# Optimization experiments

Measured on AMD Instinct MI355X. Metric: run time of the kernel, lower is better.

## Reference

```python
import jax, jax.numpy as jnp
import numpy as np

NUM_ATOMS = 50000
NUM_EDGES = 200000  # even: edges come in (fwd, rev) pairs
D_V, D_E, D_H = 133, 14, 256
DEPTH = 3


def setup_inputs() -> dict:
    key = jax.random.key(0)
    ks = jax.random.split(key, 12)
    half = NUM_EDGES // 2
    src = jax.random.randint(ks[0], (half,), 0, NUM_ATOMS)
    dst = jax.random.randint(ks[1], (half,), 0, NUM_ATOMS)
    v = jnp.concatenate([src, dst])
    w = jnp.concatenate([dst, src])
    edge_index = jnp.stack([v, w])  # [2, E]
    rev_edge_index = jnp.concatenate([jnp.arange(half) + half, jnp.arange(half)])

    def lin(k, out_d, in_d):
        return jax.random.normal(k, (out_d, in_d), jnp.float32) / np.sqrt(in_d)

    return {
        "V": jax.random.normal(ks[2], (NUM_ATOMS, D_V), jnp.float32),
        "E_feat": jax.random.normal(ks[3], (NUM_EDGES, D_E), jnp.float32),
        "edge_index": edge_index,
        "rev_edge_index": rev_edge_index,
        "Wi_atom": lin(ks[4], D_H, D_V),
        "Wi_bond": lin(ks[5], D_H, D_V + D_E),
        "Wh_atom": lin(ks[6], D_H, D_H),
        "Wh_bond": lin(ks[7], D_H, D_H),
        "Wf_atom": lin(ks[8], D_H, D_H),
        "Wf_bond": lin(ks[9], D_H, D_H),
        "Wo_atom": lin(ks[10], D_H, D_V + D_H),
    }


def _sum_and_max_into_atoms(H_e, w_idx, num_atoms):
    a_sum = jax.ops.segment_sum(H_e, w_idx, num_segments=num_atoms)
    a_max = jax.ops.segment_max(H_e, w_idx, num_segments=num_atoms)
    a_max = jnp.where(jnp.isfinite(a_max), a_max, 0.0)  # empty segments -> 0
    return a_sum, a_max


def _fuse(H, m, Wf):
    # Fusion(kind='mlp', residual=True), dropout=0:
    # residual update with a small MLP on the combined signal
    return H + jax.nn.relu((H + m) @ Wf.T)


def reference(V, E_feat, edge_index, rev_edge_index, Wi_atom, Wi_bond,
              Wh_atom, Wh_bond, Wf_atom, Wf_bond, Wo_atom):
    tau = jax.nn.relu
    num_atoms = V.shape[0]
    v = edge_index[0]
    w = edge_index[1]

    H_a = tau(V @ Wi_atom.T)                                        # [N, d_h]
    H_b = tau(jnp.concatenate([V[v], E_feat], axis=1) @ Wi_bond.T)  # [E, d_h]

    for _ in range(1, DEPTH):
        a_sum, a_max = _sum_and_max_into_atoms(H_b, w, num_atoms)
        gate = a_sum * a_max
        m_a = gate @ Wh_atom.T
        H_a = _fuse(H_a, m_a, Wf_atom)

        M_b = a_sum[v] - H_b[rev_edge_index]
        m_b = M_b @ Wh_bond.T
        H_b = _fuse(H_b, m_b, Wf_bond)

    a_sum, _ = _sum_and_max_into_atoms(H_b, w, num_atoms)
    H_atom = tau(jnp.concatenate([V, a_sum], axis=1) @ Wo_atom.T)   # [N, d_h]
    return H_atom
```

## Files before the change

### kernel.cpp

```cpp
#include <hip/hip_runtime.h>
#include <hip/hip_bf16.h>

#define NATOM 50000
#define NEDGE 200000
#define HALF  100000
#define DV    133
#define DE    14
#define DH    256
#define KVP   160
#define NBLK_SCAN ((NATOM + 255) / 256)

typedef __bf16  bf16x8 __attribute__((ext_vector_type(8)));
typedef __bf16  bf16x4 __attribute__((ext_vector_type(4)));
typedef float   f32x4  __attribute__((ext_vector_type(4)));

enum { EPI_RELU = 0, EPI_ADDBASE = 1, EPI_FUSE = 2, EPI_NONE = 3, EPI_RELUADD = 4 };
enum { AM_PLAIN = 0, AM_GATE = 1, AM_GDIFF = 2, AM_VF32 = 3, AM_XB = 4, AM_F32 = 5 };

__device__ __forceinline__ void gll16(const void* g, void* l) {
    __builtin_amdgcn_global_load_lds(
        (const __attribute__((address_space(1))) unsigned int*)g,
        (__attribute__((address_space(3))) unsigned int*)l, 16, 0, 0);
}
__device__ __forceinline__ void drain_barrier() {
    __builtin_amdgcn_s_waitcnt(0);
    __syncthreads();
}

struct GArgs {
    const __bf16* A; int lda;
    const float* asumf; const __bf16* amaxb;
    const __bf16* HbG; const int* vidx; const int* rev;
    const float* Vf; const float* Ef;
    const __bf16* W; int ldw;
    const __bf16* base; __bf16* C; float* Cf;
    int Mloc; int part0; int off0; int off1;
};

template<int AMODE, int EPI, int CLOC, int STF32, int KITERS>
__global__ __launch_bounds__(256, 2) void gemm128(GArgs g, int nblk) {
    __shared__ __bf16 Alds[4096];
    __shared__ __bf16 Blds[4096];
    const int tid  = threadIdx.x;
    const int lane = tid & 63, wv = tid >> 6;
    const int quad = lane >> 4, l16 = lane & 15;
    const int wr = (wv >> 1) * 64, wc = (wv & 1) * 64;
    const int lrow = lane >> 2, lu = lane & 3;

    for (int blk = blockIdx.x; blk < nblk; blk += gridDim.x) {
        const int ch = blk >> 1, half = blk & 1;
        const int gr0  = ch * 128;
        const int colb = half * 128;

        const int rs = tid >> 1, seg = tid & 1;
        const float *sp = nullptr; const __bf16 *hp = nullptr, *mp = nullptr;
        const float *vp = nullptr, *ep = nullptr;
        if (AMODE != AM_PLAIN) {
            int grs = gr0 + rs; if (grs > g.Mloc - 1) grs = g.Mloc - 1;
            const int maps = (grs < g.part0) ? g.off0 + grs : g.off1 + grs - g.part0;
            if (AMODE == AM_GATE)  { sp = g.asumf + (size_t)maps * DH; mp = g.amaxb + (size_t)maps * DH; }
            if (AMODE == AM_GDIFF) { sp = g.asumf + (size_t)g.vidx[maps] * DH; hp = g.HbG + (size_t)g.rev[maps] * DH; }
            if (AMODE == AM_F32)   { sp = g.asumf + (size_t)maps * DH; }
            if (AMODE == AM_VF32)  { vp = g.Vf + (size_t)maps * DV; }
            if (AMODE == AM_XB)    { vp = g.Vf + (size_t)g.vidx[maps] * DV; ep = g.Ef + (size_t)maps * DE; }
        }

        f32x4 acc[16];
#pragma unroll
        for (int i = 0; i < 16; ++i) acc[i] = (f32x4){0.f, 0.f, 0.f, 0.f};

        for (int kk = 0; kk < KITERS; ++kk) {
#pragma unroll
            for (int s = 0; s < 2; ++s) {
                int cl = (wv * 2 + s) * 16 + lrow;
                gll16(g.W + (size_t)(colb + cl) * g.ldw + kk * 32 + lu * 8,
                      Blds + (wv * 2 + s) * 512);
            }
            if (AMODE == AM_PLAIN) {
#pragma unroll
                for (int s = 0; s < 2; ++s) {
                    int r = (wv * 2 + s) * 16 + lrow;
                    int gra = gr0 + r; if (gra > g.Mloc - 1) gra = g.Mloc - 1;
                    gll16(g.A + (size_t)gra * g.lda + kk * 32 + lu * 8,
                          Alds + (wv * 2 + s) * 512);
                }
            } else {
                bf16x8 o0, o1;
                const int cb = kk * 32 + seg * 16;
                if (AMODE == AM_GATE || AMODE == AM_GDIFF || AMODE == AM_F32) {
                    f32x4 s0 = *(const f32x4*)(sp + cb);
                    f32x4 s1 = *(const f32x4*)(sp + cb + 4);
                    f32x4 s2 = *(const f32x4*)(sp + cb + 8);
                    f32x4 s3 = *(const f32x4*)(sp + cb + 12);
                    if (AMODE == AM_GATE) {
                        bf16x8 m0 = *(const bf16x8*)(mp + cb);
                        bf16x8 m1 = *(const bf16x8*)(mp + cb + 8);
#pragma unroll
                        for (int j = 0; j < 4; ++j) {
                            o0[j]     = (__bf16)(s0[j] * (float)m0[j]);
                            o0[4 + j] = (__bf16)(s1[j] * (float)m0[4 + j]);
                            o1[j]     = (__bf16)(s2[j] * (float)m1[j]);
                            o1[4 + j] = (__bf16)(s3[j] * (float)m1[4 + j]);
                        }
                    } else if (AMODE == AM_GDIFF) {
                        bf16x8 h0 = *(const bf16x8*)(hp + cb);
                        bf16x8 h1 = *(const bf16x8*)(hp + cb + 8);
#pragma unroll
                        for (int j = 0; j < 4; ++j) {
                            o0[j]     = (__bf16)(s0[j] - (float)h0[j]);
                            o0[4 + j] = (__bf16)(s1[j] - (float)h0[4 + j]);
                            o1[j]     = (__bf16)(s2[j] - (float)h1[j]);
                            o1[4 + j] = (__bf16)(s3[j] - (float)h1[4 + j]);
                        }
                    } else {
#pragma unroll
                        for (int j = 0; j < 4; ++j) {
                            o0[j]     = (__bf16)s0[j];
                            o0[4 + j] = (__bf16)s1[j];
                            o1[j]     = (__bf16)s2[j];
                            o1[4 + j] = (__bf16)s3[j];
                        }
                    }
                } else {
                    if (kk < 4) {
                        f32x4 x0, x1, x2, x3;
                        __builtin_memcpy(&x0, vp + cb, 16);
                        __builtin_memcpy(&x1, vp + cb + 4, 16);
                        __builtin_memcpy(&x2, vp + cb + 8, 16);
                        __builtin_memcpy(&x3, vp + cb + 12, 16);
#pragma unroll
                        for (int j = 0; j < 4; ++j) {
                            o0[j] = (__bf16)x0[j]; o0[4 + j] = (__bf16)x1[j];
                            o1[j] = (__bf16)x2[j]; o1[4 + j] = (__bf16)x3[j];
                        }
                    } else {
#pragma unroll
                        for (int j = 0; j < 8; ++j) {
                            int c0 = cb + j, c1 = cb + 8 + j;
                            float y0 = 0.f, y1 = 0.f;
                            if (c0 < DV) y0 = vp[c0];
                            else if (AMODE == AM_XB && c0 < DV + DE) y0 = ep[c0 - DV];
                            if (c1 < DV) y1 = vp[c1];
                            else if (AMODE == AM_XB && c1 < DV + DE) y1 = ep[c1 - DV];
                            o0[j] = (__bf16)y0; o1[j] = (__bf16)y1;
                        }
                    }
                }
                *(bf16x8*)(Alds + rs * 32 + seg * 16)     = o0;
                *(bf16x8*)(Alds + rs * 32 + seg * 16 + 8) = o1;
            }
            drain_barrier();

            bf16x8 af[4], bfv[4];
#pragma unroll
            for (int m = 0; m < 4; ++m)
                af[m] = *(const bf16x8*)(Alds + (wr + m * 16 + l16) * 32 + quad * 8);
#pragma unroll
            for (int n = 0; n < 4; ++n)
                bfv[n] = *(const bf16x8*)(Blds + (wc + n * 16 + l16) * 32 + quad * 8);
#pragma unroll
            for (int m = 0; m < 4; ++m)
#pragma unroll
                for (int n = 0; n < 4; ++n)
                    acc[m * 4 + n] = __builtin_amdgcn_mfma_f32_16x16x32_bf16(
                        af[m], bfv[n], acc[m * 4 + n], 0, 0, 0);
            drain_barrier();
        }

#pragma unroll
        for (int m = 0; m < 4; ++m)
#pragma unroll
        for (int n = 0; n < 4; ++n)
#pragma unroll
        for (int r = 0; r < 4; ++r) {
            int gr = gr0 + wr + m * 16 + quad * 4 + r;
            if (gr < g.Mloc) {
                int mapped = (gr < g.part0) ? g.off0 + gr : g.off1 + gr - g.part0;
                int crow = CLOC ? gr : mapped;
                int col = colb + wc + n * 16 + l16;
                size_t co = (size_t)crow * DH + col;
                float v = acc[m * 4 + n][r];
                float res;
                if (EPI == EPI_RELU)       res = v > 0.f ? v : 0.f;
                else if (EPI == EPI_NONE)  res = v;
                else {
                    float b = (float)g.base[(size_t)mapped * DH + col];
                    if (EPI == EPI_ADDBASE)      res = b + v;
                    else if (EPI == EPI_FUSE)    res = b + (v > 0.f ? v : 0.f);
                    else        { res = b + v; res = res > 0.f ? res : 0.f; }
                }
                if (STF32) g.Cf[co] = res;
                else       g.C[co]  = (__bf16)res;
            }
        }
    }
}

__global__ void count_deg(const int* __restrict__ widx, int* __restrict__ cnt) {
    int e = blockIdx.x * 256 + threadIdx.x;
    if (e < NEDGE) atomicAdd(&cnt[widx[e]], 1);
}

__global__ __launch_bounds__(256) void scan_p1(const int* __restrict__ cnt,
                                               int* __restrict__ rowptr,
                                               int* __restrict__ bsum) {
    __shared__ int sm[256];
    const int tid = threadIdx.x;
    const int i = blockIdx.x * 256 + tid;
    int v = (i < NATOM) ? cnt[i] : 0;
    sm[tid] = v;
    __syncthreads();
    for (int off = 1; off < 256; off <<= 1) {
        int t = (tid >= off) ? sm[tid - off] : 0;
        __syncthreads();
        sm[tid] += t;
        __syncthreads();
    }
    if (i < NATOM) rowptr[i] = sm[tid] - v;
    if (tid == 255) bsum[blockIdx.x] = sm[255];
}

__global__ __launch_bounds__(256) void scan_p2(int* __restrict__ bsum) {
    __shared__ int sm[256];
    const int tid = threadIdx.x;
    int v = (tid < NBLK_SCAN) ? bsum[tid] : 0;
    sm[tid] = v;
    __syncthreads();
    for (int off = 1; off < 256; off <<= 1) {
        int t = (tid >= off) ? sm[tid - off] : 0;
        __syncthreads();
        sm[tid] += t;
        __syncthreads();
    }
    if (tid < NBLK_SCAN) bsum[tid] = sm[tid] - v;
    if (tid == 255) bsum[NBLK_SCAN] = sm[255];
}

__global__ __launch_bounds__(256) void scan_p3(int* __restrict__ rowptr,
                                               int* __restrict__ cursor,
                                               const int* __restrict__ bsum) {
    const int i = blockIdx.x * 256 + threadIdx.x;
    if (i < NATOM) {
        int r = rowptr[i] + bsum[blockIdx.x];
        rowptr[i] = r;
        cursor[i] = r;
    }
    if (i == 0) rowptr[NATOM] = bsum[NBLK_SCAN];
}

__global__ void fill_csr(const int* __restrict__ widx, int* __restrict__ cursor,
                         int* __restrict__ eid) {
    int e = blockIdx.x * 256 + threadIdx.x;
    if (e >= NEDGE) return;
    int pos = atomicAdd(&cursor[widx[e]], 1);
    eid[pos] = e;
}

template<int WITHMAX>
__global__ __launch_bounds__(256) void seg_reduce(
    const __bf16* __restrict__ Hb, const int* __restrict__ rowptr,
    const int* __restrict__ eid,
    float* __restrict__ asum, __bf16* __restrict__ amaxb)
{
    int a = blockIdx.x * 4 + (threadIdx.x >> 6);
    if (a >= NATOM) return;
    const int lane = threadIdx.x & 63;
    const int beg = rowptr[a], end = rowptr[a + 1];
    float s0 = 0.f, s1 = 0.f, s2 = 0.f, s3 = 0.f;
    float m0 = 0.f, m1 = 0.f, m2 = 0.f, m3 = 0.f;
    for (int i = beg; i < end; ++i) {
        int e = eid[i];
        bf16x4 h = *(const bf16x4*)(Hb + (size_t)e * DH + lane * 4);
        float v0 = (float)h[0], v1 = (float)h[1], v2 = (float)h[2], v3 = (float)h[3];
        s0 += v0; s1 += v1; s2 += v2; s3 += v3;
        if (WITHMAX) {
            m0 = fmaxf(m0, v0); m1 = fmaxf(m1, v1);
            m2 = fmaxf(m2, v2); m3 = fmaxf(m3, v3);
        }
    }
    size_t o = (size_t)a * DH + lane * 4;
    *(f32x4*)(asum + o) = (f32x4){s0, s1, s2, s3};
    if (WITHMAX) {
        bf16x4 mv; mv[0] = (__bf16)m0; mv[1] = (__bf16)m1; mv[2] = (__bf16)m2; mv[3] = (__bf16)m3;
        *(bf16x4*)(amaxb + o) = mv;
    }
}

__global__ void pad_w2(const float* __restrict__ src, __bf16* __restrict__ dst,
                       int srcld, int coloff, int KS, int KD) {
    int i = blockIdx.x * 256 + threadIdx.x;
    if (i >= 256 * KD) return;
    int n = i / KD, c = i - n * KD;
    dst[i] = (c < KS) ? (__bf16)src[(size_t)n * srcld + coloff + c] : (__bf16)0.f;
}

static inline int cdiv(long a, long b) { return (int)((a + b - 1) / b); }
static inline int gsz2(int nblk) { return nblk < 2048 ? nblk : 2048; }

extern "C" void kernel_launch(void* const* d_in, const int* in_sizes, int n_in,
                              void* d_out, int out_size, void* d_ws, size_t ws_size,
                              hipStream_t stream) {
    const float* V    = (const float*)d_in[0];
    const float* Ef   = (const float*)d_in[1];
    const int*   ei   = (const int*)d_in[2];
    const int*   rev  = (const int*)d_in[3];
    const float* Wi_a = (const float*)d_in[4];
    const float* Wi_b = (const float*)d_in[5];
    const float* Wh_a = (const float*)d_in[6];
    const float* Wh_b = (const float*)d_in[7];
    const float* Wf_a = (const float*)d_in[8];
    const float* Wf_b = (const float*)d_in[9];
    const float* Wo   = (const float*)d_in[10];
    float* out = (float*)d_out;

    const int* vidx = ei;
    const int* widx = ei + NEDGE;

    char* ws = (char*)d_ws;
    __bf16* Hb    = (__bf16*)(ws + 0);
    __bf16* Ha    = (__bf16*)(ws + 102400000);
    char*   S     = ws + 128000000;
    float*  asum  = (float*)(ws + 192000000);
    __bf16* amaxb = (__bf16*)(S + 0);
    __bf16* Ta    = (__bf16*)(S + 25600000);
    __bf16* Tb    = (__bf16*)(S + 0);
    __bf16* T     = (__bf16*)(S + 25600000);
    __bf16* Wia   = (__bf16*)(ws + 243200000);
    __bf16* Wib   = (__bf16*)(ws + 243281920);
    __bf16* Wo1   = (__bf16*)(ws + 243363840);
    __bf16* Wo2   = (__bf16*)(ws + 243445760);
    __bf16* Wha   = (__bf16*)(ws + 243576832);
    __bf16* Whb   = (__bf16*)(ws + 243707904);
    __bf16* Wfa   = (__bf16*)(ws + 243838976);
    __bf16* Wfb   = (__bf16*)(ws + 243970048);
    int*  rowptr  = (int*)(ws + 244101120);
    int*  cursor  = (int*)(ws + 244301312);
    int*  eid     = (int*)(ws + 244501504);
    int*  bsum    = (int*)(ws + 128000000);
    (void)ws_size;

    hipMemsetAsync(cursor, 0, NATOM * sizeof(int), stream);
    count_deg<<<cdiv(NEDGE, 256), 256, 0, stream>>>(widx, cursor);
    scan_p1<<<NBLK_SCAN, 256, 0, stream>>>(cursor, rowptr, bsum);
    scan_p2<<<1, 256, 0, stream>>>(bsum);
    scan_p3<<<NBLK_SCAN, 256, 0, stream>>>(rowptr, cursor, bsum);
    fill_csr<<<cdiv(NEDGE, 256), 256, 0, stream>>>(widx, cursor, eid);

    pad_w2<<<cdiv(256 * KVP, 256), 256, 0, stream>>>(Wi_a, Wia, DV, 0, DV, KVP);
    pad_w2<<<cdiv(256 * KVP, 256), 256, 0, stream>>>(Wi_b, Wib, DV + DE, 0, DV + DE, KVP);
    pad_w2<<<cdiv(256 * KVP, 256), 256, 0, stream>>>(Wo, Wo1, DV + DH, 0, DV, KVP);
    pad_w2<<<cdiv(256 * DH, 256), 256, 0, stream>>>(Wo, Wo2, DV + DH, DV, DH, DH);
    pad_w2<<<cdiv(256 * DH, 256), 256, 0, stream>>>(Wh_a, Wha, DH, 0, DH, DH);
    pad_w2<<<cdiv(256 * DH, 256), 256, 0, stream>>>(Wh_b, Whb, DH, 0, DH, DH);
    pad_w2<<<cdiv(256 * DH, 256), 256, 0, stream>>>(Wf_a, Wfa, DH, 0, DH, DH);
    pad_w2<<<cdiv(256 * DH, 256), 256, 0, stream>>>(Wf_b, Wfb, DH, 0, DH, DH);

    GArgs ga{};
    ga.asumf = asum; ga.amaxb = amaxb; ga.HbG = Hb; ga.vidx = vidx; ga.rev = rev;
    ga.Vf = V; ga.Ef = Ef;

    {
        int nblk = cdiv(NATOM, 128) * 2;
        ga.W = Wia; ga.ldw = KVP; ga.C = Ha;
        ga.Mloc = NATOM; ga.part0 = NATOM; ga.off0 = 0; ga.off1 = 0;
        gemm128<AM_VF32, EPI_RELU, 0, 0, 5><<<gsz2(nblk), 256, 0, stream>>>(ga, nblk);
    }
    {
        int nblk = cdiv(NEDGE, 128) * 2;
        ga.W = Wib; ga.ldw = KVP; ga.C = Hb;
        ga.Mloc = NEDGE; ga.part0 = NEDGE; ga.off0 = 0; ga.off1 = 0;
        gemm128<AM_XB, EPI_RELU, 0, 0, 5><<<gsz2(nblk), 256, 0, stream>>>(ga, nblk);
    }

    for (int it = 0; it < 2; ++it) {
        seg_reduce<1><<<cdiv(NATOM, 4), 256, 0, stream>>>(Hb, rowptr, eid, asum, amaxb);

        {
            int nblk = cdiv(NATOM, 128) * 2;
            ga.W = Wha; ga.ldw = DH; ga.base = Ha; ga.C = Ta;
            ga.Mloc = NATOM; ga.part0 = NATOM; ga.off0 = 0; ga.off1 = 0;
            gemm128<AM_GATE, EPI_ADDBASE, 1, 0, 8><<<gsz2(nblk), 256, 0, stream>>>(ga, nblk);
            ga.A = Ta; ga.lda = DH; ga.W = Wfa; ga.base = Ha; ga.C = Ha;
            gemm128<AM_PLAIN, EPI_FUSE, 0, 0, 8><<<gsz2(nblk), 256, 0, stream>>>(ga, nblk);
        }

        for (int c = 0; c < 2; ++c) {
            int nblk = cdiv(HALF, 128) * 2;
            ga.W = Whb; ga.ldw = DH; ga.base = Hb; ga.C = Tb;
            ga.Mloc = HALF; ga.part0 = HALF / 2; ga.off0 = c * 50000; ga.off1 = HALF + c * 50000;
            gemm128<AM_GDIFF, EPI_ADDBASE, 1, 0, 8><<<gsz2(nblk), 256, 0, stream>>>(ga, nblk);
            ga.A = Tb; ga.lda = DH; ga.W = Wfb; ga.base = Hb; ga.C = Hb;
            gemm128<AM_PLAIN, EPI_FUSE, 0, 0, 8><<<gsz2(nblk), 256, 0, stream>>>(ga, nblk);
        }
    }

    seg_reduce<0><<<cdiv(NATOM, 4), 256, 0, stream>>>(Hb, rowptr, eid, asum, nullptr);
    {
        int nblk = cdiv(NATOM, 128) * 2;
        ga.Mloc = NATOM; ga.part0 = NATOM; ga.off0 = 0; ga.off1 = 0;
        ga.W = Wo1; ga.ldw = KVP; ga.C = T;
        gemm128<AM_VF32, EPI_NONE, 0, 0, 5><<<gsz2(nblk), 256, 0, stream>>>(ga, nblk);
        ga.W = Wo2; ga.ldw = DH; ga.base = T; ga.Cf = out;
        gemm128<AM_F32, EPI_RELUADD, 0, 1, 8><<<gsz2(nblk), 256, 0, stream>>>(ga, nblk);
    }
}
```

Measured before the change: 1.206 ms.

## Widen GEMM tile to full 256 output columns with 512-thread blocks

The GEMM kernel now uses 512-thread blocks that compute a 128x256 tile, covering every output column, instead of two 128x128 half tiles per row chunk. Each A row is therefore gathered and converted once rather than twice, which halves the redundant gather/gate/diff work and the A-side global traffic. The cost is a larger B shared-memory tile and bigger blocks, which may lower occupancy and leave fewer blocks to spread across the GPU.

New measurement: 1.204 ms. About the same (-0.1%).

```diff
diff --git a/kernel.cpp b/kernel.cpp
--- a/kernel.cpp
+++ b/kernel.cpp
@@ -38,21 +38,19 @@
 };
 
 template<int AMODE, int EPI, int CLOC, int STF32, int KITERS>
-__global__ __launch_bounds__(256, 2) void gemm128(GArgs g, int nblk) {
+__global__ __launch_bounds__(512, 2) void gemmk(GArgs g, int nblk) {
     __shared__ __bf16 Alds[4096];
-    __shared__ __bf16 Blds[4096];
+    __shared__ __bf16 Blds[8192];
     const int tid  = threadIdx.x;
     const int lane = tid & 63, wv = tid >> 6;
     const int quad = lane >> 4, l16 = lane & 15;
-    const int wr = (wv >> 1) * 64, wc = (wv & 1) * 64;
+    const int wr = (wv >> 2) * 64, wc = (wv & 3) * 64;
     const int lrow = lane >> 2, lu = lane & 3;
 
     for (int blk = blockIdx.x; blk < nblk; blk += gridDim.x) {
-        const int ch = blk >> 1, half = blk & 1;
-        const int gr0  = ch * 128;
-        const int colb = half * 128;
-
-        const int rs = tid >> 1, seg = tid & 1;
+        const int gr0 = blk * 128;
+
+        const int rs = tid >> 2, seg = tid & 3;
         const float *sp = nullptr; const __bf16 *hp = nullptr, *mp = nullptr;
         const float *vp = nullptr, *ep = nullptr;
         if (AMODE != AM_PLAIN) {
@@ -73,81 +71,62 @@
 #pragma unroll
             for (int s = 0; s < 2; ++s) {
                 int cl = (wv * 2 + s) * 16 + lrow;
-                gll16(g.W + (size_t)(colb + cl) * g.ldw + kk * 32 + lu * 8,
+                gll16(g.W + (size_t)cl * g.ldw + kk * 32 + lu * 8,
                       Blds + (wv * 2 + s) * 512);
             }
             if (AMODE == AM_PLAIN) {
-#pragma unroll
-                for (int s = 0; s < 2; ++s) {
-                    int r = (wv * 2 + s) * 16 + lrow;
-                    int gra = gr0 + r; if (gra > g.Mloc - 1) gra = g.Mloc - 1;
-                    gll16(g.A + (size_t)gra * g.lda + kk * 32 + lu * 8,
-                          Alds + (wv * 2 + s) * 512);
-                }
+                int r = wv * 16 + lrow;
+                int gra = gr0 + r; if (gra > g.Mloc - 1) gra = g.Mloc - 1;
+                gll16(g.A + (size_t)gra * g.lda + kk * 32 + lu * 8,
+                      Alds + wv * 512);
             } else {
-                bf16x8 o0, o1;
-                const int cb = kk * 32 + seg * 16;
+                bf16x8 o0;
+                const int cb = kk * 32 + seg * 8;
                 if (AMODE == AM_GATE || AMODE == AM_GDIFF || AMODE == AM_F32) {
                     f32x4 s0 = *(const f32x4*)(sp + cb);
                     f32x4 s1 = *(const f32x4*)(sp + cb + 4);
-                    f32x4 s2 = *(const f32x4*)(sp + cb + 8);
-                    f32x4 s3 = *(const f32x4*)(sp + cb + 12);
                     if (AMODE == AM_GATE) {
                         bf16x8 m0 = *(const bf16x8*)(mp + cb);
-                        bf16x8 m1 = *(const bf16x8*)(mp + cb + 8);
 #pragma unroll
                         for (int j = 0; j < 4; ++j) {
                             o0[j]     = (__bf16)(s0[j] * (float)m0[j]);
                             o0[4 + j] = (__bf16)(s1[j] * (float)m0[4 + j]);
-                            o1[j]     = (__bf16)(s2[j] * (float)m1[j]);
-                            o1[4 + j] = (__bf16)(s3[j] * (float)m1[4 + j]);
                         }
                     } else if (AMODE == AM_GDIFF) {
                         bf16x8 h0 = *(const bf16x8*)(hp + cb);
-                        bf16x8 h1 = *(const bf16x8*)(hp + cb + 8);
 #pragma unroll
                         for (int j = 0; j < 4; ++j) {
                             o0[j]     = (__bf16)(s0[j] - (float)h0[j]);
                             o0[4 + j] = (__bf16)(s1[j] - (float)h0[4 + j]);
-                            o1[j]     = (__bf16)(s2[j] - (float)h1[j]);
-                            o1[4 + j] = (__bf16)(s3[j] - (float)h1[4 + j]);
                         }
                     } else {
 #pragma unroll
                         for (int j = 0; j < 4; ++j) {
                             o0[j]     = (__bf16)s0[j];
                             o0[4 + j] = (__bf16)s1[j];
-                            o1[j]     = (__bf16)s2[j];
-                            o1[4 + j] = (__bf16)s3[j];
                         }
                     }
                 } else {
                     if (kk < 4) {
-                        f32x4 x0, x1, x2, x3;
+                        f32x4 x0, x1;
                         __builtin_memcpy(&x0, vp + cb, 16);
                         __builtin_memcpy(&x1, vp + cb + 4, 16);
-                        __builtin_memcpy(&x2, vp + cb + 8, 16);
-                        __builtin_memcpy(&x3, vp + cb + 12, 16);
 #pragma unroll
                         for (int j = 0; j < 4; ++j) {
                             o0[j] = (__bf16)x0[j]; o0[4 + j] = (__bf16)x1[j];
-                            o1[j] = (__bf16)x2[j]; o1[4 + j] = (__bf16)x3[j];
                         }
                     } else {
 #pragma unroll
                         for (int j = 0; j < 8; ++j) {
-                            int c0 = cb + j, c1 = cb + 8 + j;
-                            float y0 = 0.f, y1 = 0.f;
+                            int c0 = cb + j;
+                            float y0 = 0.f;
                             if (c0 < DV) y0 = vp[c0];
                             else if (AMODE == AM_XB && c0 < DV + DE) y0 = ep[c0 - DV];
-                            if (c1 < DV) y1 = vp[c1];
-                            else if (AMODE == AM_XB && c1 < DV + DE) y1 = ep[c1 - DV];
-                            o0[j] = (__bf16)y0; o1[j] = (__bf16)y1;
+                            o0[j] = (__bf16)y0;
                         }
                     }
                 }
-                *(bf16x8*)(Alds + rs * 32 + seg * 16)     = o0;
-                *(bf16x8*)(Alds + rs * 32 + seg * 16 + 8) = o1;
+                *(bf16x8*)(Alds + rs * 32 + seg * 8) = o0;
             }
             drain_barrier();
 
@@ -177,7 +156,7 @@
             if (gr < g.Mloc) {
                 int mapped = (gr < g.part0) ? g.off0 + gr : g.off1 + gr - g.part0;
                 int crow = CLOC ? gr : mapped;
-                int col = colb + wc + n * 16 + l16;
+                int col = wc + n * 16 + l16;
                 size_t co = (size_t)crow * DH + col;
                 float v = acc[m * 4 + n][r];
                 float res;
@@ -360,47 +339,47 @@
     ga.Vf = V; ga.Ef = Ef;
 
     {
-        int nblk = cdiv(NATOM, 128) * 2;
+        int nblk = cdiv(NATOM, 128);
         ga.W = Wia; ga.ldw = KVP; ga.C = Ha;
         ga.Mloc = NATOM; ga.part0 = NATOM; ga.off0 = 0; ga.off1 = 0;
-        gemm128<AM_VF32, EPI_RELU, 0, 0, 5><<<gsz2(nblk), 256, 0, stream>>>(ga, nblk);
+        gemmk<AM_VF32, EPI_RELU, 0, 0, 5><<<gsz2(nblk), 512, 0, stream>>>(ga, nblk);
     }
     {
-        int nblk = cdiv(NEDGE, 128) * 2;
+        int nblk = cdiv(NEDGE, 128);
         ga.W = Wib; ga.ldw = KVP; ga.C = Hb;
         ga.Mloc = NEDGE; ga.part0 = NEDGE; ga.off0 = 0; ga.off1 = 0;
-        gemm128<AM_XB, EPI_RELU, 0, 0, 5><<<gsz2(nblk), 256, 0, stream>>>(ga, nblk);
+        gemmk<AM_XB, EPI_RELU, 0, 0, 5><<<gsz2(nblk), 512, 0, stream>>>(ga, nblk);
     }
 
     for (int it = 0; it < 2; ++it) {
         seg_reduce<1><<<cdiv(NATOM, 4), 256, 0, stream>>>(Hb, rowptr, eid, asum, amaxb);
 
         {
-            int nblk = cdiv(NATOM, 128) * 2;
+            int nblk = cdiv(NATOM, 128);
             ga.W = Wha; ga.ldw = DH; ga.base = Ha; ga.C = Ta;
             ga.Mloc = NATOM; ga.part0 = NATOM; ga.off0 = 0; ga.off1 = 0;
-            gemm128<AM_GATE, EPI_ADDBASE, 1, 0, 8><<<gsz2(nblk), 256, 0, stream>>>(ga, nblk);
+            gemmk<AM_GATE, EPI_ADDBASE, 1, 0, 8><<<gsz2(nblk), 512, 0, stream>>>(ga, nblk);
             ga.A = Ta; ga.lda = DH; ga.W = Wfa; ga.base = Ha; ga.C = Ha;
-            gemm128<AM_PLAIN, EPI_FUSE, 0, 0, 8><<<gsz2(nblk), 256, 0, stream>>>(ga, nblk);
+            gemmk<AM_PLAIN, EPI_FUSE, 0, 0, 8><<<gsz2(nblk), 512, 0, stream>>>(ga, nblk);
         }
 
         for (int c = 0; c < 2; ++c) {
-            int nblk = cdiv(HALF, 128) * 2;
+            int nblk = cdiv(HALF, 128);
             ga.W = Whb; ga.ldw = DH; ga.base = Hb; ga.C = Tb;
             ga.Mloc = HALF; ga.part0 = HALF / 2; ga.off0 = c * 50000; ga.off1 = HALF + c * 50000;
-            gemm128<AM_GDIFF, EPI_ADDBASE, 1, 0, 8><<<gsz2(nblk), 256, 0, stream>>>(ga, nblk);
+            gemmk<AM_GDIFF, EPI_ADDBASE, 1, 0, 8><<<gsz2(nblk), 512, 0, stream>>>(ga, nblk);
             ga.A = Tb; ga.lda = DH; ga.W = Wfb; ga.base = Hb; ga.C = Hb;
-            gemm128<AM_PLAIN, EPI_FUSE, 0, 0, 8><<<gsz2(nblk), 256, 0, stream>>>(ga, nblk);
+            gemmk<AM_PLAIN, EPI_FUSE, 0, 0, 8><<<gsz2(nblk), 512, 0, stream>>>(ga, nblk);
         }
     }
 
     seg_reduce<0><<<cdiv(NATOM, 4), 256, 0, stream>>>(Hb, rowptr, eid, asum, nullptr);
     {
-        int nblk = cdiv(NATOM, 128) * 2;
+        int nblk = cdiv(NATOM, 128);
         ga.Mloc = NATOM; ga.part0 = NATOM; ga.off0 = 0; ga.off1 = 0;
         ga.W = Wo1; ga.ldw = KVP; ga.C = T;
-        gemm128<AM_VF32, EPI_NONE, 0, 0, 5><<<gsz2(nblk), 256, 0, stream>>>(ga, nblk);
+        gemmk<AM_VF32, EPI_NONE, 0, 0, 5><<<gsz2(nblk), 512, 0, stream>>>(ga, nblk);
         ga.W = Wo2; ga.ldw = DH; ga.base = T; ga.Cf = out;
-        gemm128<AM_F32, EPI_RELUADD, 0, 1, 8><<<gsz2(nblk), 256, 0, stream>>>(ga, nblk);
-    }
-}
+        gemmk<AM_F32, EPI_RELUADD, 0, 1, 8><<<gsz2(nblk), 512, 0, stream>>>(ga, nblk);
+    }
+}
```
